# Optimization experiments

Measured on AMD Instinct MI355X. Metric: run time of the kernel, lower is better.

## Reference

```python
import jax, jax.numpy as jnp
import numpy as np

B, S, H = 4, 4096, 2048
E = 64          # num_routed_experts
TOP_K = 8
TEMP = 1.0      # router_temperature


def setup_inputs() -> dict:
    key = jax.random.key(0)
    k1, k2 = jax.random.split(key)
    hidden_states = jax.random.normal(k1, (B, S, H), dtype=jnp.float32)
    # nn.Linear weight: [out_features, in_features] = [E, H]
    gate_w = jax.random.normal(k2, (E, H), dtype=jnp.float32) * (1.0 / np.sqrt(H))
    return {"hidden_states": hidden_states, "gate_w": gate_w}


def reference(hidden_states, gate_w):
    # Gate projection + temperature scaling: [B,S,H] @ [H,E] -> [B,S,E]
    router_logits = jnp.einsum("bsh,eh->bse", hidden_states, gate_w) / TEMP
    # Top-k over experts
    routing_weights, selected_experts = jax.lax.top_k(router_logits, TOP_K)
    # Softmax over the top-k slots in fp32, cast back to input dtype
    routing_weights = jax.nn.softmax(routing_weights.astype(jnp.float32), axis=-1).astype(hidden_states.dtype)
    return router_logits, routing_weights, selected_experts
```

## Files before the change

kernel.cpp:

```cpp
#include <hip/hip_runtime.h>
#include <math.h>

#define HH 2048
#define EE 64
#define TOPK 8
#define NT 16384
#define MT 32
#define KC 16
#define KQR 512
#define NCH 32
#define LS 68

typedef __attribute__((ext_vector_type(8)))  short short8;
typedef __attribute__((ext_vector_type(16))) float f32x16;

static __device__ __forceinline__ void cvt3(const float4& a, const float4& b,
                                            short8& h, short8& m, short8& l)
{
    const float v[8] = {a.x, a.y, a.z, a.w, b.x, b.y, b.z, b.w};
#pragma unroll
    for (int i = 0; i < 8; ++i) {
        const unsigned int u = __float_as_uint(v[i]);
        h[i] = (short)(u >> 16);
        const float r1 = v[i] - __uint_as_float(u & 0xffff0000u);
        const unsigned int u1 = __float_as_uint(r1);
        m[i] = (short)(u1 >> 16);
        const float r2 = r1 - __uint_as_float(u1 & 0xffff0000u);
        const unsigned int u2 = __float_as_uint(r2);
        l[i] = (short)((u2 + 0x7fffu + ((u2 >> 16) & 1u)) >> 16);
    }
}

__global__ __launch_bounds__(256, 2) void router_fused(
    const float* __restrict__ x,
    const float* __restrict__ w,
    float* __restrict__ out_logits,
    float* __restrict__ out_wts,
    float* __restrict__ out_idx)
{
    __shared__ float slog[MT * LS];

    const int t    = threadIdx.x;
    const int wv   = t >> 6;
    const int lane = t & 63;
    const int kq   = wv;
    const int l5   = lane >> 5;
    const int lr   = lane & 31;
    const int tok0 = blockIdx.x * MT;

    const float* xp  = x + (size_t)(tok0 + lr) * HH + kq * KQR + l5 * 8;
    const float* wp0 = w + (size_t)(lr)      * HH + kq * KQR + l5 * 8;
    const float* wp1 = w + (size_t)(32 + lr) * HH + kq * KQR + l5 * 8;

    f32x16 accM0 = {0}, accM1 = {0};
    f32x16 accS0 = {0}, accS1 = {0};

    struct Chunk { float4 x0, x1, a0, a1, b0, b1; };
    Chunk S0, S1, S2, S3;

    auto load = [&](Chunk& s, int c) {
        const int o = c * KC;
        s.x0 = *(const float4*)(xp  + o);
        s.x1 = *(const float4*)(xp  + o + 4);
        s.a0 = *(const float4*)(wp0 + o);
        s.a1 = *(const float4*)(wp0 + o + 4);
        s.b0 = *(const float4*)(wp1 + o);
        s.b1 = *(const float4*)(wp1 + o + 4);
    };

    auto compute = [&](const Chunk& s) {
        short8 xh, xm, xl;
        cvt3(s.x0, s.x1, xh, xm, xl);
        {
            short8 bh, bm, bl;
            cvt3(s.a0, s.a1, bh, bm, bl);
            accM0 = __builtin_amdgcn_mfma_f32_32x32x16_bf16(xh, bh, accM0, 0, 0, 0);
            accS0 = __builtin_amdgcn_mfma_f32_32x32x16_bf16(xh, bm, accS0, 0, 0, 0);
            accS0 = __builtin_amdgcn_mfma_f32_32x32x16_bf16(xm, bh, accS0, 0, 0, 0);
            accS0 = __builtin_amdgcn_mfma_f32_32x32x16_bf16(xh, bl, accS0, 0, 0, 0);
            accS0 = __builtin_amdgcn_mfma_f32_32x32x16_bf16(xl, bh, accS0, 0, 0, 0);
            accS0 = __builtin_amdgcn_mfma_f32_32x32x16_bf16(xm, bm, accS0, 0, 0, 0);
        }
        {
            short8 bh, bm, bl;
            cvt3(s.b0, s.b1, bh, bm, bl);
            accM1 = __builtin_amdgcn_mfma_f32_32x32x16_bf16(xh, bh, accM1, 0, 0, 0);
            accS1 = __builtin_amdgcn_mfma_f32_32x32x16_bf16(xh, bm, accS1, 0, 0, 0);
            accS1 = __builtin_amdgcn_mfma_f32_32x32x16_bf16(xm, bh, accS1, 0, 0, 0);
            accS1 = __builtin_amdgcn_mfma_f32_32x32x16_bf16(xh, bl, accS1, 0, 0, 0);
            accS1 = __builtin_amdgcn_mfma_f32_32x32x16_bf16(xl, bh, accS1, 0, 0, 0);
            accS1 = __builtin_amdgcn_mfma_f32_32x32x16_bf16(xm, bm, accS1, 0, 0, 0);
        }
    };

    load(S0, 0); load(S1, 1); load(S2, 2); load(S3, 3);

#pragma unroll 1
    for (int c = 0; c < NCH; c += 4) {
        compute(S0); if (c + 4 < NCH) load(S0, c + 4);
        compute(S1); if (c + 5 < NCH) load(S1, c + 5);
        compute(S2); if (c + 6 < NCH) load(S2, c + 6);
        compute(S3); if (c + 7 < NCH) load(S3, c + 7);
    }

#pragma unroll 1
    for (int q = 0; q < 4; ++q) {
        if (kq == q) {
#pragma unroll
            for (int eb = 0; eb < 2; ++eb) {
                const f32x16& AM = eb ? accM1 : accM0;
                const f32x16& AS = eb ? accS1 : accS0;
                const int col = eb * 32 + lr;
#pragma unroll
                for (int r = 0; r < 16; ++r) {
                    const int row = (r & 3) + 8 * (r >> 2) + 4 * l5;
                    const float val = AM[r] + AS[r];
                    if (q == 0) slog[row * LS + col] = val;
                    else        slog[row * LS + col] += val;
                }
            }
        }
        __syncthreads();
    }

    {
        const int row = t >> 3;
        const int c8  = (t & 7) * 8;
        const float4 o0 = *(const float4*)&slog[row * LS + c8];
        const float4 o1 = *(const float4*)&slog[row * LS + c8 + 4];
        float* dst = out_logits + (size_t)(tok0 + row) * EE + c8;
        *(float4*)dst       = o0;
        *(float4*)(dst + 4) = o1;
    }

    if (t < MT) {
        float tv[TOPK];
        int   ti[TOPK];
#pragma unroll
        for (int q = 0; q < TOPK; ++q) { tv[q] = -INFINITY; ti[q] = 0; }

        for (int e = 0; e < EE; ++e) {
            const float val = slog[t * LS + e];
            if (val > tv[TOPK - 1]) {
                tv[TOPK - 1] = val;
                ti[TOPK - 1] = e;
#pragma unroll
                for (int q = TOPK - 1; q > 0; --q) {
                    if (tv[q] > tv[q - 1]) {
                        float fv = tv[q]; tv[q] = tv[q - 1]; tv[q - 1] = fv;
                        int   fi = ti[q]; ti[q] = ti[q - 1]; ti[q - 1] = fi;
                    }
                }
            }
        }

        const float m = tv[0];
        float ew[TOPK];
        float sum = 0.f;
#pragma unroll
        for (int q = 0; q < TOPK; ++q) { ew[q] = expf(tv[q] - m); sum += ew[q]; }
        const float inv = 1.f / sum;

        const size_t tok = (size_t)(tok0 + t);
        float4 w0, w1, i0, i1;
        w0.x = ew[0] * inv; w0.y = ew[1] * inv; w0.z = ew[2] * inv; w0.w = ew[3] * inv;
        w1.x = ew[4] * inv; w1.y = ew[5] * inv; w1.z = ew[6] * inv; w1.w = ew[7] * inv;
        i0.x = (float)ti[0]; i0.y = (float)ti[1]; i0.z = (float)ti[2]; i0.w = (float)ti[3];
        i1.x = (float)ti[4]; i1.y = (float)ti[5]; i1.z = (float)ti[6]; i1.w = (float)ti[7];
        *(float4*)(out_wts + tok * TOPK)     = w0;
        *(float4*)(out_wts + tok * TOPK + 4) = w1;
        *(float4*)(out_idx + tok * TOPK)     = i0;
        *(float4*)(out_idx + tok * TOPK + 4) = i1;
    }
}

extern "C" void kernel_launch(void* const* d_in, const int* in_sizes, int n_in,
                              void* d_out, int out_size, void* d_ws, size_t ws_size,
                              hipStream_t stream) {
    const float* x = (const float*)d_in[0];
    const float* w = (const float*)d_in[1];
    float* out        = (float*)d_out;
    float* out_logits = out;
    float* out_wts    = out + (size_t)NT * EE;
    float* out_idx    = out_wts + (size_t)NT * TOPK;

    hipLaunchKernelGGL(router_fused, dim3(NT / MT), dim3(256), 0, stream,
                       x, w, out_logits, out_wts, out_idx);
}
```

Baseline: 231.9 us.

## Pre-split gate weights into bf16x3 MFMA layout and double waves per block

```diff
diff --git a/kernel.cpp b/kernel.cpp
--- a/kernel.cpp
+++ b/kernel.cpp
@@ -31,9 +31,31 @@
     }
 }
 
-__global__ __launch_bounds__(256, 2) void router_fused(
+__global__ __launch_bounds__(256) void wsplit(
+    const float* __restrict__ w, short* __restrict__ wsw)
+{
+    const int e = blockIdx.x;
+    const int o = threadIdx.x;
+    const int k = o * 8;
+    const float4 a = *(const float4*)(w + (size_t)e * HH + k);
+    const float4 b = *(const float4*)(w + (size_t)e * HH + k + 4);
+    short8 h, m, l;
+    cvt3(a, b, h, m, l);
+
+    const int eb = e >> 5, lr = e & 31;
+    const int kq = k >> 9;
+    const int c  = (k >> 4) & 31;
+    const int l5 = (k >> 3) & 1;
+    const int lane = l5 * 32 + lr;
+    short* dst = wsw + ((size_t)(((eb * 4 + kq) * 32 + c) * 3) * 64 + lane) * 8;
+    *(short8*)(dst)            = h;
+    *(short8*)(dst + 64 * 8)   = m;
+    *(short8*)(dst + 128 * 8)  = l;
+}
+
+__global__ __launch_bounds__(512, 4) void router_fused(
     const float* __restrict__ x,
-    const float* __restrict__ w,
+    const short* __restrict__ wsw,
     float* __restrict__ out_logits,
     float* __restrict__ out_wts,
     float* __restrict__ out_idx)
@@ -43,94 +65,72 @@
     const int t    = threadIdx.x;
     const int wv   = t >> 6;
     const int lane = t & 63;
-    const int kq   = wv;
+    const int eb   = wv & 1;
+    const int kq   = wv >> 1;
     const int l5   = lane >> 5;
     const int lr   = lane & 31;
     const int tok0 = blockIdx.x * MT;
 
-    const float* xp  = x + (size_t)(tok0 + lr) * HH + kq * KQR + l5 * 8;
-    const float* wp0 = w + (size_t)(lr)      * HH + kq * KQR + l5 * 8;
-    const float* wp1 = w + (size_t)(32 + lr) * HH + kq * KQR + l5 * 8;
+    const float* xp = x + (size_t)(tok0 + lr) * HH + kq * KQR + l5 * 8;
+    const short* wbase = wsw + ((size_t)((eb * 4 + kq) * 32) * 192 + lane) * 8;
 
-    f32x16 accM0 = {0}, accM1 = {0};
-    f32x16 accS0 = {0}, accS1 = {0};
+    f32x16 accM = {0}, accS = {0};
 
-    struct Chunk { float4 x0, x1, a0, a1, b0, b1; };
-    Chunk S0, S1, S2, S3;
+    short8 wA[3], wB[3];
+    float4 xa0, xa1, xb0, xb1;
 
-    auto load = [&](Chunk& s, int c) {
-        const int o = c * KC;
-        s.x0 = *(const float4*)(xp  + o);
-        s.x1 = *(const float4*)(xp  + o + 4);
-        s.a0 = *(const float4*)(wp0 + o);
-        s.a1 = *(const float4*)(wp0 + o + 4);
-        s.b0 = *(const float4*)(wp1 + o);
-        s.b1 = *(const float4*)(wp1 + o + 4);
+    auto wload = [&](short8* bw, int c) {
+        const short* p0 = wbase + (size_t)c * 1536;
+        bw[0] = *(const short8*)(p0);
+        bw[1] = *(const short8*)(p0 + 512);
+        bw[2] = *(const short8*)(p0 + 1024);
+    };
+    auto xload = [&](float4& a, float4& b, int c) {
+        a = *(const float4*)(xp + c * KC);
+        b = *(const float4*)(xp + c * KC + 4);
+    };
+    auto compute = [&](const float4& a, const float4& b, const short8* bw) {
+        short8 xh, xm, xl;
+        cvt3(a, b, xh, xm, xl);
+        accM = __builtin_amdgcn_mfma_f32_32x32x16_bf16(xh, bw[0], accM, 0, 0, 0);
+        accS = __builtin_amdgcn_mfma_f32_32x32x16_bf16(xh, bw[1], accS, 0, 0, 0);
+        accS = __builtin_amdgcn_mfma_f32_32x32x16_bf16(xm, bw[0], accS, 0, 0, 0);
+        accS = __builtin_amdgcn_mfma_f32_32x32x16_bf16(xh, bw[2], accS, 0, 0, 0);
+        accS = __builtin_amdgcn_mfma_f32_32x32x16_bf16(xl, bw[0], accS, 0, 0, 0);
+        accS = __builtin_amdgcn_mfma_f32_32x32x16_bf16(xm, bw[1], accS, 0, 0, 0);
     };
 
-    auto compute = [&](const Chunk& s) {
-        short8 xh, xm, xl;
-        cvt3(s.x0, s.x1, xh, xm, xl);
-        {
-            short8 bh, bm, bl;
-            cvt3(s.a0, s.a1, bh, bm, bl);
-            accM0 = __builtin_amdgcn_mfma_f32_32x32x16_bf16(xh, bh, accM0, 0, 0, 0);
-            accS0 = __builtin_amdgcn_mfma_f32_32x32x16_bf16(xh, bm, accS0, 0, 0, 0);
-            accS0 = __builtin_amdgcn_mfma_f32_32x32x16_bf16(xm, bh, accS0, 0, 0, 0);
-            accS0 = __builtin_amdgcn_mfma_f32_32x32x16_bf16(xh, bl, accS0, 0, 0, 0);
-            accS0 = __builtin_amdgcn_mfma_f32_32x32x16_bf16(xl, bh, accS0, 0, 0, 0);
-            accS0 = __builtin_amdgcn_mfma_f32_32x32x16_bf16(xm, bm, accS0, 0, 0, 0);
-        }
-        {
-            short8 bh, bm, bl;
-            cvt3(s.b0, s.b1, bh, bm, bl);
-            accM1 = __builtin_amdgcn_mfma_f32_32x32x16_bf16(xh, bh, accM1, 0, 0, 0);
-            accS1 = __builtin_amdgcn_mfma_f32_32x32x16_bf16(xh, bm, accS1, 0, 0, 0);
-            accS1 = __builtin_amdgcn_mfma_f32_32x32x16_bf16(xm, bh, accS1, 0, 0, 0);
-            accS1 = __builtin_amdgcn_mfma_f32_32x32x16_bf16(xh, bl, accS1, 0, 0, 0);
-            accS1 = __builtin_amdgcn_mfma_f32_32x32x16_bf16(xl, bh, accS1, 0, 0, 0);
-            accS1 = __builtin_amdgcn_mfma_f32_32x32x16_bf16(xm, bm, accS1, 0, 0, 0);
-        }
-    };
-
-    load(S0, 0); load(S1, 1); load(S2, 2); load(S3, 3);
+    wload(wA, 0); xload(xa0, xa1, 0);
+    wload(wB, 1); xload(xb0, xb1, 1);
 
 #pragma unroll 1
-    for (int c = 0; c < NCH; c += 4) {
-        compute(S0); if (c + 4 < NCH) load(S0, c + 4);
-        compute(S1); if (c + 5 < NCH) load(S1, c + 5);
-        compute(S2); if (c + 6 < NCH) load(S2, c + 6);
-        compute(S3); if (c + 7 < NCH) load(S3, c + 7);
+    for (int c = 0; c < NCH; c += 2) {
+        compute(xa0, xa1, wA);
+        if (c + 2 < NCH) { wload(wA, c + 2); xload(xa0, xa1, c + 2); }
+        compute(xb0, xb1, wB);
+        if (c + 3 < NCH) { wload(wB, c + 3); xload(xb0, xb1, c + 3); }
     }
 
+    const int col = eb * 32 + lr;
 #pragma unroll 1
     for (int q = 0; q < 4; ++q) {
         if (kq == q) {
 #pragma unroll
-            for (int eb = 0; eb < 2; ++eb) {
-                const f32x16& AM = eb ? accM1 : accM0;
-                const f32x16& AS = eb ? accS1 : accS0;
-                const int col = eb * 32 + lr;
-#pragma unroll
-                for (int r = 0; r < 16; ++r) {
-                    const int row = (r & 3) + 8 * (r >> 2) + 4 * l5;
-                    const float val = AM[r] + AS[r];
-                    if (q == 0) slog[row * LS + col] = val;
-                    else        slog[row * LS + col] += val;
-                }
+            for (int r = 0; r < 16; ++r) {
+                const int row = (r & 3) + 8 * (r >> 2) + 4 * l5;
+                const float val = accM[r] + accS[r];
+                if (q == 0) slog[row * LS + col] = val;
+                else        slog[row * LS + col] += val;
             }
         }
         __syncthreads();
     }
 
     {
-        const int row = t >> 3;
-        const int c8  = (t & 7) * 8;
-        const float4 o0 = *(const float4*)&slog[row * LS + c8];
-        const float4 o1 = *(const float4*)&slog[row * LS + c8 + 4];
-        float* dst = out_logits + (size_t)(tok0 + row) * EE + c8;
-        *(float4*)dst       = o0;
-        *(float4*)(dst + 4) = o1;
+        const int row = t >> 4;
+        const int c4  = (t & 15) * 4;
+        const float4 o0 = *(const float4*)&slog[row * LS + c4];
+        *(float4*)(out_logits + (size_t)(tok0 + row) * EE + c4) = o0;
     }
 
     if (t < MT) {
@@ -183,7 +183,9 @@
     float* out_logits = out;
     float* out_wts    = out + (size_t)NT * EE;
     float* out_idx    = out_wts + (size_t)NT * TOPK;
+    short* wsw = (short*)d_ws;
 
-    hipLaunchKernelGGL(router_fused, dim3(NT / MT), dim3(256), 0, stream,
-                       x, w, out_logits, out_wts, out_idx);
+    hipLaunchKernelGGL(wsplit, dim3(EE), dim3(256), 0, stream, w, wsw);
+    hipLaunchKernelGGL(router_fused, dim3(NT / MT), dim3(512), 0, stream,
+                       x, wsw, out_logits, out_wts, out_idx);
 }
```

After: 233.8 us. No clear change (+0.8%).
